# Kernel optimization log

Measured on AMD Instinct MI355X. Metric: run time of the kernel, lower is better.

## Reference

```python
import jax, jax.numpy as jnp
import numpy as np
from jax import lax

NUM_STEPS = 20
BATCH, DIM, HID = 4096, 512, 2048


def setup_inputs() -> dict:
    key = jax.random.key(0)
    k_z, k_w1, k_w2 = jax.random.split(key, 3)
    z0 = jax.random.normal(k_z, (BATCH, DIM), dtype=jnp.float32)
    # fan-in scaled weights so the ODE dynamics stay well-conditioned
    W1 = jax.random.normal(k_w1, (DIM + 1, HID), dtype=jnp.float32) * (1.0 / np.sqrt(DIM + 1))
    b1 = jnp.zeros((HID,), dtype=jnp.float32)
    W2 = jax.random.normal(k_w2, (HID, DIM), dtype=jnp.float32) * (0.1 / np.sqrt(HID))
    b2 = jnp.zeros((DIM,), dtype=jnp.float32)
    t0 = jnp.zeros((), dtype=jnp.float32)
    t1 = jnp.ones((), dtype=jnp.float32)
    return {"z0": z0, "W1": W1, "b1": b1, "W2": W2, "b2": b2, "t0": t0, "t1": t1}


def reference(z0, W1, b1, W2, b2, t0, t1):
    h = (t1 - t0) / NUM_STEPS

    def func(z, t):
        # time broadcast to [batch, 1], concatenated to the state (Neural-ODE MLP dynamics)
        tb = jnp.full((z.shape[0], 1), t, dtype=z.dtype)
        hidden = jnp.tanh(jnp.concatenate([z, tb], axis=-1) @ W1 + b1)
        return hidden @ W2 + b2

    def step(z, i):
        t = t0 + i * h
        k1 = func(z, t)
        k2 = func(z + 0.5 * h * k1, t + 0.5 * h)
        k3 = func(z + 0.5 * h * k2, t + 0.5 * h)
        k4 = func(z + h * k3, t + h)
        z_next = z + (h / 6.0) * (k1 + 2.0 * k2 + 2.0 * k3 + k4)
        return z_next, None

    z, _ = lax.scan(step, z0, jnp.arange(NUM_STEPS, dtype=z0.dtype))
    return z
```

## Files before the change

### kernel.cpp

```cpp
#include <hip/hip_runtime.h>
#include <hip/hip_bf16.h>

#define BATCH 4096
#define DIM   512
#define HID   2048
#define NSTEPS 20

typedef __attribute__((ext_vector_type(8))) short short8;
typedef __attribute__((ext_vector_type(4))) short short4v;
typedef __attribute__((ext_vector_type(4))) float floatx4;

#define GLL(dst, src) __builtin_amdgcn_global_load_lds( \
    (const __attribute__((address_space(1))) void*)(src), \
    (__attribute__((address_space(3))) void*)(dst), 16, 0, 0)

__device__ __forceinline__ short f2bf(float x) {
    union { float f; unsigned u; } v; v.f = x;
    unsigned r = v.u + 0x7fffu + ((v.u >> 16) & 1u);
    return (short)(r >> 16);
}

__device__ __forceinline__ float fast_tanh(float x) {
    float e = __builtin_amdgcn_exp2f(x * 2.8853900817779268f);
    float r = __builtin_amdgcn_rcpf(1.0f + e);
    return 1.0f - 2.0f * r;
}

__global__ void transpose_cvt(const float* __restrict__ src, short* __restrict__ dst,
                              int K, int N) {
    __shared__ float tile[32][33];
    int k0 = blockIdx.x * 32, n0 = blockIdx.y * 32;
    int tx = threadIdx.x, ty = threadIdx.y;
    #pragma unroll
    for (int r = ty; r < 32; r += 8)
        tile[r][tx] = src[(size_t)(k0 + r) * N + n0 + tx];
    __syncthreads();
    #pragma unroll
    for (int r = ty; r < 32; r += 8)
        dst[(size_t)(n0 + r) * K + k0 + tx] = f2bf(tile[tx][r]);
}

__global__ void extract_row(const float* __restrict__ W1, float* __restrict__ w1last) {
    int i = blockIdx.x * 256 + threadIdx.x;
    w1last[i] = W1[(size_t)DIM * HID + i];
}

__global__ void init_abuf(const float* __restrict__ z0, short* __restrict__ abuf) {
    size_t i = (size_t)(blockIdx.x * 256 + threadIdx.x) * 4;
    float4 zv = *(const float4*)(z0 + i);
    short4v o;
    o[0] = f2bf(zv.x); o[1] = f2bf(zv.y); o[2] = f2bf(zv.z); o[3] = f2bf(zv.w);
    *(short4v*)(abuf + i) = o;
}

__global__ __launch_bounds__(256, 2)
void gemm1_tanh(const short* __restrict__ A, const short* __restrict__ Bt,
                const float* __restrict__ b1, const float* __restrict__ w1last,
                const float* __restrict__ t0p, const float* __restrict__ t1p,
                float c_t, float step_i,
                short* __restrict__ hidden) {
    __shared__ short Alds[2][128 * 64];
    __shared__ short Blds[2][128 * 64];
    const int tid = threadIdx.x;
    const int lane = tid & 63;
    const int wave = tid >> 6;
    const int wm = wave >> 1, wn = wave & 1;
    const int bm0 = blockIdx.x * 128;
    const int bn0 = blockIdx.y * 128;

    const float t0 = t0p[0], t1 = t1p[0];
    const float h = (t1 - t0) / (float)NSTEPS;
    const float teval = t0 + (step_i + c_t) * h;

    floatx4 acc[4][4];
    #pragma unroll
    for (int i = 0; i < 4; i++)
        #pragma unroll
        for (int j = 0; j < 4; j++) acc[i][j] = (floatx4)0.f;

    const int fr = lane & 15;
    const int fkc = lane >> 4;
    const int rx = fr & 7;

    auto stage = [&](int it, int bufi) {
        const int kk = it * 64;
        #pragma unroll
        for (int p = 0; p < 4; p++) {
            int c = tid + p * 256;
            int row = c >> 3;
            int g = (c & 7) ^ (row & 7);
            GLL(&Alds[bufi][c * 8], A  + (size_t)(bm0 + row) * DIM + kk + g * 8);
            GLL(&Blds[bufi][c * 8], Bt + (size_t)(bn0 + row) * DIM + kk + g * 8);
        }
    };

    stage(0, 0);
    for (int it = 0; it < 8; ++it) {
        __syncthreads();
        if (it < 7) stage(it + 1, (it + 1) & 1);
        const short* Ab = Alds[it & 1];
        const short* Bb = Blds[it & 1];
        #pragma unroll
        for (int s = 0; s < 2; s++) {
            const int slot = ((s * 4 + fkc) ^ rx) * 8;
            short8 af[4], bfr[4];
            #pragma unroll
            for (int mt = 0; mt < 4; mt++)
                af[mt] = *(const short8*)&Ab[(wm * 64 + mt * 16 + fr) * 64 + slot];
            #pragma unroll
            for (int nt = 0; nt < 4; nt++)
                bfr[nt] = *(const short8*)&Bb[(wn * 64 + nt * 16 + fr) * 64 + slot];
            #pragma unroll
            for (int mt = 0; mt < 4; mt++)
                #pragma unroll
                for (int nt = 0; nt < 4; nt++)
                    acc[mt][nt] = __builtin_amdgcn_mfma_f32_16x16x32_bf16(bfr[nt], af[mt], acc[mt][nt], 0, 0, 0);
        }
    }
    #pragma unroll
    for (int mt = 0; mt < 4; mt++) {
        int m = bm0 + wm * 64 + mt * 16 + fr;
        short* hrow = hidden + (size_t)m * HID;
        #pragma unroll
        for (int nt = 0; nt < 4; nt++) {
            int n0 = bn0 + wn * 64 + nt * 16 + fkc * 4;
            float4 bb = *(const float4*)&b1[n0];
            float4 wl = *(const float4*)&w1last[n0];
            short4v o;
            o[0] = f2bf(fast_tanh(acc[mt][nt][0] + bb.x + teval * wl.x));
            o[1] = f2bf(fast_tanh(acc[mt][nt][1] + bb.y + teval * wl.y));
            o[2] = f2bf(fast_tanh(acc[mt][nt][2] + bb.z + teval * wl.z));
            o[3] = f2bf(fast_tanh(acc[mt][nt][3] + bb.w + teval * wl.w));
            *(short4v*)&hrow[n0] = o;
        }
    }
}

__global__ __launch_bounds__(256, 2)
void gemm2_fused(const short* __restrict__ hidden,
                 const short* __restrict__ Bt,
                 const float* __restrict__ b2,
                 float* __restrict__ z,
                 float* __restrict__ kacc, short* __restrict__ abuf,
                 const float* __restrict__ t0p, const float* __restrict__ t1p,
                 int mode, float wk, float alpha_c) {
    __shared__ short lds[32768];
    const int tid = threadIdx.x;
    const int lane = tid & 63;
    const int wave = tid >> 6;
    const int bm0 = blockIdx.x * 64;
    const int bn0 = blockIdx.y * 64;
    const int kbase = wave * 512;
    short* wbase = &lds[wave * 8192];

    const int fr = lane & 15;
    const int fkc = lane >> 4;
    const int l2r = lane >> 2;
    const int lch = lane & 3;

    floatx4 acc[4][4];
    #pragma unroll
    for (int i = 0; i < 4; i++)
        #pragma unroll
        for (int j = 0; j < 4; j++) acc[i][j] = (floatx4)0.f;

    auto issue = [&](int it, int bufi) {
        short* sA = wbase + bufi * 4096;
        short* sB = sA + 2048;
        const int k0 = kbase + it * 32;
        #pragma unroll
        for (int j = 0; j < 4; j++) {
            int row = j * 16 + l2r;
            GLL(&sA[j * 512 + lane * 8], hidden + (size_t)(bm0 + row) * HID + k0 + lch * 8);
            GLL(&sB[j * 512 + lane * 8], Bt     + (size_t)(bn0 + row) * HID + k0 + lch * 8);
        }
    };

    issue(0, 0);
    for (int it = 0; it < 16; ++it) {
        __syncthreads();
        if (it < 15) issue(it + 1, (it + 1) & 1);
        const short* sA = wbase + (it & 1) * 4096;
        const short* sB = sA + 2048;
        short8 af[4], bfr[4];
        #pragma unroll
        for (int mt = 0; mt < 4; mt++)
            af[mt] = *(const short8*)&sA[(mt * 16 + fr) * 32 + fkc * 8];
        #pragma unroll
        for (int nt = 0; nt < 4; nt++)
            bfr[nt] = *(const short8*)&sB[(nt * 16 + fr) * 32 + fkc * 8];
        #pragma unroll
        for (int mt = 0; mt < 4; mt++)
            #pragma unroll
            for (int nt = 0; nt < 4; nt++)
                acc[mt][nt] = __builtin_amdgcn_mfma_f32_16x16x32_bf16(af[mt], bfr[nt], acc[mt][nt], 0, 0, 0);
    }

    __syncthreads();
    float* fslab = (float*)wbase;
    #pragma unroll
    for (int mt = 0; mt < 4; mt++)
        #pragma unroll
        for (int nt = 0; nt < 4; nt++)
            #pragma unroll
            for (int r = 0; r < 4; r++) {
                int row = mt * 16 + fkc * 4 + r;
                int col = nt * 16 + fr;
                fslab[row * 64 + col] = acc[mt][nt][r];
            }
    __syncthreads();

    const int rrow = tid >> 2;
    const int cb = (tid & 3) * 16;
    float4 v[4];
    #pragma unroll
    for (int ch = 0; ch < 4; ch++) v[ch] = make_float4(0.f, 0.f, 0.f, 0.f);
    #pragma unroll
    for (int w = 0; w < 4; w++) {
        const float* fs = (const float*)&lds[w * 8192];
        #pragma unroll
        for (int ch = 0; ch < 4; ch++) {
            float4 p = *(const float4*)&fs[rrow * 64 + cb + ch * 4];
            v[ch].x += p.x; v[ch].y += p.y; v[ch].z += p.z; v[ch].w += p.w;
        }
    }

    const float h = (t1p[0] - t0p[0]) / (float)NSTEPS;
    const float ah = alpha_c * h;
    const float h6 = h / 6.0f;
    const size_t base = (size_t)(bm0 + rrow) * DIM + bn0 + cb;
    #pragma unroll
    for (int ch = 0; ch < 4; ch++) {
        float4 bb = *(const float4*)&b2[bn0 + cb + ch * 4];
        float kv[4] = { v[ch].x + bb.x, v[ch].y + bb.y, v[ch].z + bb.z, v[ch].w + bb.w };
        size_t idx = base + ch * 4;
        float4 zv = *(const float4*)&z[idx];
        float zn[4];
        if (mode == 0) {
            *(float4*)&kacc[idx] = make_float4(kv[0], kv[1], kv[2], kv[3]);
            zn[0] = zv.x + ah * kv[0]; zn[1] = zv.y + ah * kv[1];
            zn[2] = zv.z + ah * kv[2]; zn[3] = zv.w + ah * kv[3];
        } else if (mode == 1) {
            float4 ka = *(const float4*)&kacc[idx];
            *(float4*)&kacc[idx] = make_float4(ka.x + wk * kv[0], ka.y + wk * kv[1],
                                               ka.z + wk * kv[2], ka.w + wk * kv[3]);
            zn[0] = zv.x + ah * kv[0]; zn[1] = zv.y + ah * kv[1];
            zn[2] = zv.z + ah * kv[2]; zn[3] = zv.w + ah * kv[3];
        } else {
            float4 ka = *(const float4*)&kacc[idx];
            zn[0] = zv.x + h6 * (ka.x + kv[0]); zn[1] = zv.y + h6 * (ka.y + kv[1]);
            zn[2] = zv.z + h6 * (ka.z + kv[2]); zn[3] = zv.w + h6 * (ka.w + kv[3]);
            *(float4*)&z[idx] = make_float4(zn[0], zn[1], zn[2], zn[3]);
        }
        short4v o;
        o[0] = f2bf(zn[0]); o[1] = f2bf(zn[1]); o[2] = f2bf(zn[2]); o[3] = f2bf(zn[3]);
        *(short4v*)&abuf[idx] = o;
    }
}

extern "C" void kernel_launch(void* const* d_in, const int* in_sizes, int n_in,
                              void* d_out, int out_size, void* d_ws, size_t ws_size,
                              hipStream_t stream) {
    const float* z0  = (const float*)d_in[0];
    const float* W1  = (const float*)d_in[1];
    const float* b1  = (const float*)d_in[2];
    const float* W2  = (const float*)d_in[3];
    const float* b2  = (const float*)d_in[4];
    const float* t0p = (const float*)d_in[5];
    const float* t1p = (const float*)d_in[6];
    float* z = (float*)d_out;

    char* ws = (char*)d_ws;
    short* W1t    = (short*)(ws);
    short* W2t    = (short*)(ws + (2u << 20));
    float* w1last = (float*)(ws + (4u << 20));
    short* abuf   = (short*)(ws + (4u << 20) + (1u << 16));
    short* hidden = (short*)(ws + (8u << 20) + (1u << 16));
    float* kacc   = (float*)(ws + (24u << 20) + (1u << 16));

    hipMemcpyAsync(z, z0, (size_t)BATCH * DIM * sizeof(float),
                   hipMemcpyDeviceToDevice, stream);
    transpose_cvt<<<dim3(DIM / 32, HID / 32), dim3(32, 8), 0, stream>>>(W1, W1t, DIM, HID);
    transpose_cvt<<<dim3(HID / 32, DIM / 32), dim3(32, 8), 0, stream>>>(W2, W2t, HID, DIM);
    extract_row<<<HID / 256, 256, 0, stream>>>(W1, w1last);
    init_abuf<<<BATCH * DIM / 4 / 256, 256, 0, stream>>>(z0, abuf);

    const dim3 g1(BATCH / 128, HID / 128), g2(BATCH / 64, DIM / 64), b(256);
    for (int i = 0; i < NSTEPS; i++) {
        float fi = (float)i;
        gemm1_tanh<<<g1, b, 0, stream>>>(abuf, W1t, b1, w1last, t0p, t1p, 0.0f, fi, hidden);
        gemm2_fused<<<g2, b, 0, stream>>>(hidden, W2t, b2, z, kacc, abuf, t0p, t1p, 0, 1.0f, 0.5f);
        gemm1_tanh<<<g1, b, 0, stream>>>(abuf, W1t, b1, w1last, t0p, t1p, 0.5f, fi, hidden);
        gemm2_fused<<<g2, b, 0, stream>>>(hidden, W2t, b2, z, kacc, abuf, t0p, t1p, 1, 2.0f, 0.5f);
        gemm1_tanh<<<g1, b, 0, stream>>>(abuf, W1t, b1, w1last, t0p, t1p, 0.5f, fi, hidden);
        gemm2_fused<<<g2, b, 0, stream>>>(hidden, W2t, b2, z, kacc, abuf, t0p, t1p, 1, 2.0f, 1.0f);
        gemm1_tanh<<<g1, b, 0, stream>>>(abuf, W1t, b1, w1last, t0p, t1p, 1.0f, fi, hidden);
        gemm2_fused<<<g2, b, 0, stream>>>(hidden, W2t, b2, z, kacc, abuf, t0p, t1p, 2, 1.0f, 0.0f);
    }
}
```

Before: 3.605 ms.

## Load MFMA operands directly from global memory instead of LDS staging

Both GEMM kernels drop the double-buffered global_load_lds staging and have each wave read its MFMA fragments straight from global memory into registers, relying on L1/L2 for reuse. gemm1 changes its tiling so each wave owns a 64x64 tile, with the block covering 256 rows by 64 columns. gemm2 keeps LDS only for the cross-wave split-K reduction. The aim is to remove LDS traffic and barriers, at the cost of more redundant global/cache traffic and less explicit overlap of loads with MFMA work.

```diff
diff --git a/kernel.cpp b/kernel.cpp
--- a/kernel.cpp
+++ b/kernel.cpp
@@ -9,10 +9,6 @@
 typedef __attribute__((ext_vector_type(8))) short short8;
 typedef __attribute__((ext_vector_type(4))) short short4v;
 typedef __attribute__((ext_vector_type(4))) float floatx4;
-
-#define GLL(dst, src) __builtin_amdgcn_global_load_lds( \
-    (const __attribute__((address_space(1))) void*)(src), \
-    (__attribute__((address_space(3))) void*)(dst), 16, 0, 0)
 
 __device__ __forceinline__ short f2bf(float x) {
     union { float f; unsigned u; } v; v.f = x;
@@ -54,19 +50,19 @@
 }
 
 __global__ __launch_bounds__(256, 2)
-void gemm1_tanh(const short* __restrict__ A, const short* __restrict__ Bt,
+void gemm1_tanh(const short* __restrict__ A,
+                const short* __restrict__ Bt,
                 const float* __restrict__ b1, const float* __restrict__ w1last,
                 const float* __restrict__ t0p, const float* __restrict__ t1p,
                 float c_t, float step_i,
                 short* __restrict__ hidden) {
-    __shared__ short Alds[2][128 * 64];
-    __shared__ short Blds[2][128 * 64];
     const int tid = threadIdx.x;
     const int lane = tid & 63;
     const int wave = tid >> 6;
-    const int wm = wave >> 1, wn = wave & 1;
-    const int bm0 = blockIdx.x * 128;
-    const int bn0 = blockIdx.y * 128;
+    const int bm0 = blockIdx.x * 256 + wave * 64;
+    const int bn0 = blockIdx.y * 64;
+    const int fr = lane & 15;
+    const int fkc = lane >> 4;
 
     const float t0 = t0p[0], t1 = t1p[0];
     const float h = (t1 - t0) / (float)NSTEPS;
@@ -78,52 +74,37 @@
         #pragma unroll
         for (int j = 0; j < 4; j++) acc[i][j] = (floatx4)0.f;
 
-    const int fr = lane & 15;
-    const int fkc = lane >> 4;
-    const int rx = fr & 7;
-
-    auto stage = [&](int it, int bufi) {
-        const int kk = it * 64;
-        #pragma unroll
-        for (int p = 0; p < 4; p++) {
-            int c = tid + p * 256;
-            int row = c >> 3;
-            int g = (c & 7) ^ (row & 7);
-            GLL(&Alds[bufi][c * 8], A  + (size_t)(bm0 + row) * DIM + kk + g * 8);
-            GLL(&Blds[bufi][c * 8], Bt + (size_t)(bn0 + row) * DIM + kk + g * 8);
-        }
-    };
-
-    stage(0, 0);
-    for (int it = 0; it < 8; ++it) {
-        __syncthreads();
-        if (it < 7) stage(it + 1, (it + 1) & 1);
-        const short* Ab = Alds[it & 1];
-        const short* Bb = Blds[it & 1];
-        #pragma unroll
-        for (int s = 0; s < 2; s++) {
-            const int slot = ((s * 4 + fkc) ^ rx) * 8;
-            short8 af[4], bfr[4];
-            #pragma unroll
-            for (int mt = 0; mt < 4; mt++)
-                af[mt] = *(const short8*)&Ab[(wm * 64 + mt * 16 + fr) * 64 + slot];
-            #pragma unroll
-            for (int nt = 0; nt < 4; nt++)
-                bfr[nt] = *(const short8*)&Bb[(wn * 64 + nt * 16 + fr) * 64 + slot];
+    const short* Ab = A  + (size_t)(bm0 + fr) * DIM + fkc * 8;
+    const short* Bb = Bt + (size_t)(bn0 + fr) * DIM + fkc * 8;
+
+    #pragma unroll
+    for (int kk = 0; kk < DIM; kk += 64) {
+        short8 af[4][2], bfr[4][2];
+        #pragma unroll
+        for (int mt = 0; mt < 4; mt++) {
+            af[mt][0] = *(const short8*)(Ab + (size_t)mt * 16 * DIM + kk);
+            af[mt][1] = *(const short8*)(Ab + (size_t)mt * 16 * DIM + kk + 32);
+        }
+        #pragma unroll
+        for (int nt = 0; nt < 4; nt++) {
+            bfr[nt][0] = *(const short8*)(Bb + (size_t)nt * 16 * DIM + kk);
+            bfr[nt][1] = *(const short8*)(Bb + (size_t)nt * 16 * DIM + kk + 32);
+        }
+        #pragma unroll
+        for (int s = 0; s < 2; s++)
             #pragma unroll
             for (int mt = 0; mt < 4; mt++)
                 #pragma unroll
                 for (int nt = 0; nt < 4; nt++)
-                    acc[mt][nt] = __builtin_amdgcn_mfma_f32_16x16x32_bf16(bfr[nt], af[mt], acc[mt][nt], 0, 0, 0);
-        }
+                    acc[mt][nt] = __builtin_amdgcn_mfma_f32_16x16x32_bf16(bfr[nt][s], af[mt][s], acc[mt][nt], 0, 0, 0);
     }
     #pragma unroll
     for (int mt = 0; mt < 4; mt++) {
-        int m = bm0 + wm * 64 + mt * 16 + fr;
+        int m = bm0 + mt * 16 + fr;
         short* hrow = hidden + (size_t)m * HID;
         #pragma unroll
         for (int nt = 0; nt < 4; nt++) {
-            int n0 = bn0 + wn * 64 + nt * 16 + fkc * 4;
+            int n0 = bn0 + nt * 16 + fkc * 4;
             float4 bb = *(const float4*)&b1[n0];
             float4 wl = *(const float4*)&w1last[n0];
             short4v o;
@@ -144,19 +125,15 @@
                  float* __restrict__ kacc, short* __restrict__ abuf,
                  const float* __restrict__ t0p, const float* __restrict__ t1p,
                  int mode, float wk, float alpha_c) {
-    __shared__ short lds[32768];
+    __shared__ float red[4 * 4096];
     const int tid = threadIdx.x;
     const int lane = tid & 63;
     const int wave = tid >> 6;
     const int bm0 = blockIdx.x * 64;
     const int bn0 = blockIdx.y * 64;
     const int kbase = wave * 512;
-    short* wbase = &lds[wave * 8192];
-
     const int fr = lane & 15;
     const int fkc = lane >> 4;
-    const int l2r = lane >> 2;
-    const int lch = lane & 3;
 
     floatx4 acc[4][4];
     #pragma unroll
@@ -164,40 +141,32 @@
         #pragma unroll
         for (int j = 0; j < 4; j++) acc[i][j] = (floatx4)0.f;
 
-    auto issue = [&](int it, int bufi) {
-        short* sA = wbase + bufi * 4096;
-        short* sB = sA + 2048;
-        const int k0 = kbase + it * 32;
-        #pragma unroll
-        for (int j = 0; j < 4; j++) {
-            int row = j * 16 + l2r;
-            GLL(&sA[j * 512 + lane * 8], hidden + (size_t)(bm0 + row) * HID + k0 + lch * 8);
-            GLL(&sB[j * 512 + lane * 8], Bt     + (size_t)(bn0 + row) * HID + k0 + lch * 8);
-        }
-    };
-
-    issue(0, 0);
-    for (int it = 0; it < 16; ++it) {
-        __syncthreads();
-        if (it < 15) issue(it + 1, (it + 1) & 1);
-        const short* sA = wbase + (it & 1) * 4096;
-        const short* sB = sA + 2048;
-        short8 af[4], bfr[4];
-        #pragma unroll
-        for (int mt = 0; mt < 4; mt++)
-            af[mt] = *(const short8*)&sA[(mt * 16 + fr) * 32 + fkc * 8];
-        #pragma unroll
-        for (int nt = 0; nt < 4; nt++)
-            bfr[nt] = *(const short8*)&sB[(nt * 16 + fr) * 32 + fkc * 8];
-        #pragma unroll
-        for (int mt = 0; mt < 4; mt++)
+    const short* Ab = hidden + (size_t)(bm0 + fr) * HID + kbase + fkc * 8;
+    const short* Bb = Bt     + (size_t)(bn0 + fr) * HID + kbase + fkc * 8;
+
+    #pragma unroll
+    for (int kk = 0; kk < 512; kk += 64) {
+        short8 af[4][2], bfr[4][2];
+        #pragma unroll
+        for (int mt = 0; mt < 4; mt++) {
+            af[mt][0] = *(const short8*)(Ab + (size_t)mt * 16 * HID + kk);
+            af[mt][1] = *(const short8*)(Ab + (size_t)mt * 16 * HID + kk + 32);
+        }
+        #pragma unroll
+        for (int nt = 0; nt < 4; nt++) {
+            bfr[nt][0] = *(const short8*)(Bb + (size_t)nt * 16 * HID + kk);
+            bfr[nt][1] = *(const short8*)(Bb + (size_t)nt * 16 * HID + kk + 32);
+        }
+        #pragma unroll
+        for (int s = 0; s < 2; s++)
             #pragma unroll
-            for (int nt = 0; nt < 4; nt++)
-                acc[mt][nt] = __builtin_amdgcn_mfma_f32_16x16x32_bf16(af[mt], bfr[nt], acc[mt][nt], 0, 0, 0);
-    }
-
-    __syncthreads();
-    float* fslab = (float*)wbase;
+            for (int mt = 0; mt < 4; mt++)
+                #pragma unroll
+                for (int nt = 0; nt < 4; nt++)
+                    acc[mt][nt] = __builtin_amdgcn_mfma_f32_16x16x32_bf16(af[mt][s], bfr[nt][s], acc[mt][nt], 0, 0, 0);
+    }
+
+    float* fslab = &red[wave * 4096];
     #pragma unroll
     for (int mt = 0; mt < 4; mt++)
         #pragma unroll
@@ -217,7 +186,7 @@
     for (int ch = 0; ch < 4; ch++) v[ch] = make_float4(0.f, 0.f, 0.f, 0.f);
     #pragma unroll
     for (int w = 0; w < 4; w++) {
-        const float* fs = (const float*)&lds[w * 8192];
+        const float* fs = &red[w * 4096];
         #pragma unroll
         for (int ch = 0; ch < 4; ch++) {
             float4 p = *(const float4*)&fs[rrow * 64 + cb + ch * 4];
@@ -285,7 +254,7 @@
     extract_row<<<HID / 256, 256, 0, stream>>>(W1, w1last);
     init_abuf<<<BATCH * DIM / 4 / 256, 256, 0, stream>>>(z0, abuf);
 
-    const dim3 g1(BATCH / 128, HID / 128), g2(BATCH / 64, DIM / 64), b(256);
+    const dim3 g1(BATCH / 256, HID / 64), g2(BATCH / 64, DIM / 64), b(256);
     for (int i = 0; i < NSTEPS; i++) {
         float fi = (float)i;
         gemm1_tanh<<<g1, b, 0, stream>>>(abuf, W1t, b1, w1last, t0p, t1p, 0.0f, fi, hidden);
```

New measurement: 6.396 ms. 1.77x slower.
